# Performance work log

Hardware: AMD Instinct MI355X
Metric: run time of the kernel (lower is better)

The kernel has to match this reference:

```python
import jax, jax.numpy as jnp
import numpy as np

BN_EPS = 1e-5
TN_EPS = 1e-4


def binarize(x):
    # Clipped straight-through binarization (Courbariaux BNN / Brevitas 1-bit):
    # forward = sign(x) in {-1,+1}, backward = hardtanh STE.
    xc = jnp.clip(x, -1.0, 1.0)
    return xc + jax.lax.stop_gradient(jnp.where(x >= 0, 1.0, -1.0).astype(x.dtype) - xc)


def setup_inputs() -> dict:
    key = jax.random.key(0)
    ks = jax.random.split(key, 20)
    B, D, H, C = 16384, 1024, 1024, 10
    inp = {"x": jax.random.uniform(ks[0], (B, D), dtype=jnp.float32)}
    dims = [(H, D), (H, H), (H, H), (C, H)]
    for i, (o, n) in enumerate(dims):
        inp[f"W{i+1}"] = jax.random.uniform(ks[1 + i], (o, n), minval=-1.0, maxval=1.0, dtype=jnp.float32)
    # BatchNorm1d params (eval mode, running stats) for the 3 hidden layers
    for i in range(3):
        k0, k1, k2, k3 = jax.random.split(ks[5 + i], 4)
        inp[f"g{i+1}"] = 1.0 + 0.1 * jax.random.normal(k0, (H,), dtype=jnp.float32)
        inp[f"b{i+1}"] = 0.1 * jax.random.normal(k1, (H,), dtype=jnp.float32)
        inp[f"m{i+1}"] = 0.1 * jax.random.normal(k2, (H,), dtype=jnp.float32)
        inp[f"v{i+1}"] = 0.5 + jax.random.uniform(k3, (H,), dtype=jnp.float32)
    # TensorNorm (scalar norm on the logits)
    inp["tn_w"] = jnp.ones((), dtype=jnp.float32)
    inp["tn_b"] = jnp.zeros((), dtype=jnp.float32)
    inp["tn_m"] = jnp.zeros((), dtype=jnp.float32)
    inp["tn_v"] = jnp.ones((), dtype=jnp.float32)
    return inp


def reference(x, W1, W2, W3, W4,
              g1, b1, m1, v1,
              g2, b2, m2, v2,
              g3, b3, m3, v3,
              tn_w, tn_b, tn_m, tn_v):
    h = binarize(2.0 * x.reshape(x.shape[0], -1) - 1.0)
    # Dropout is identity in eval mode.
    bn = [(g1, b1, m1, v1), (g2, b2, m2, v2), (g3, b3, m3, v3)]
    for W, (g, b, m, v) in zip((W1, W2, W3), bn):
        h = h @ binarize(W).T                      # [B,H] fake-quant linear, no bias
        h = (h - m) * (g * jax.lax.rsqrt(v + BN_EPS)) + b  # BatchNorm1d eval
        h = binarize(h)                            # 1-bit activation quant
    h = h @ binarize(W4).T                         # [B,10]
    # TensorNorm: scalar affine normalization over the whole tensor
    return (h - tn_m) * jax.lax.rsqrt(tn_v + TN_EPS) * tn_w + tn_b
```

## Files before the change

### kernel.cpp

```cpp
#include <hip/hip_runtime.h>
#include <stdint.h>

typedef int  v4i  __attribute__((ext_vector_type(4)));
typedef int  v16i __attribute__((ext_vector_type(16)));
typedef unsigned int uint32;

#define BATCH 16384
#define FEAT  1024

#define OFF_ACTA 0u
#define OFF_ACTB 16777216u
#define OFF_WA1  33554432u
#define OFF_WA2  34603008u
#define OFF_WA3  35651584u
#define OFF_WA4  36700160u
#define OFF_TH   36732928u

__global__ void __launch_bounds__(256) prep_kernel(
    const float* __restrict__ x,
    const float* __restrict__ W1, const float* __restrict__ W2,
    const float* __restrict__ W3, const float* __restrict__ W4,
    const float* __restrict__ g1, const float* __restrict__ b1,
    const float* __restrict__ m1, const float* __restrict__ v1,
    const float* __restrict__ g2, const float* __restrict__ b2,
    const float* __restrict__ m2, const float* __restrict__ v2,
    const float* __restrict__ g3, const float* __restrict__ b3,
    const float* __restrict__ m3, const float* __restrict__ v3,
    char* __restrict__ actA, char* __restrict__ wa1, char* __restrict__ wa2,
    char* __restrict__ wa3, char* __restrict__ wa4, int* __restrict__ TH)
{
    int b = blockIdx.x;
    if (b == 609) {
        for (int gid = threadIdx.x; gid < 3072; gid += 256) {
            int l = gid >> 10, j = gid & 1023;
            const float *g, *bb, *m, *v;
            if (l == 0)      { g = g1; bb = b1; m = m1; v = v1; }
            else if (l == 1) { g = g2; bb = b2; m = m2; v = v2; }
            else             { g = g3; bb = b3; m = m3; v = v3; }
            double gd = (double)g[j], bd = (double)bb[j], md = (double)m[j], vd = (double)v[j];
            double s = gd / sqrt(vd + 1e-5);
            int t2;
            if (s > 0.0)      t2 = (int)ceil(md - bd / s);
            else if (s < 0.0) t2 = -(int)floor(md - bd / s);
            else              t2 = (bd >= 0.0) ? -2000000 : 2000000;
            TH[gid] = t2;
        }
        return;
    }

    const float* src; char* dst; float thr; int nrows; int dblk;
    const float* gp = nullptr;
    if (b < 512)      { src = x  + (size_t)b * 32768;            dst = actA; dblk = b;      thr = 0.5f; nrows = 32; }
    else if (b < 544) { int mb = b - 512; src = W1 + (size_t)mb * 32768; dst = wa1; dblk = mb; thr = 0.0f; nrows = 32; gp = g1; }
    else if (b < 576) { int mb = b - 544; src = W2 + (size_t)mb * 32768; dst = wa2; dblk = mb; thr = 0.0f; nrows = 32; gp = g2; }
    else if (b < 608) { int mb = b - 576; src = W3 + (size_t)mb * 32768; dst = wa3; dblk = mb; thr = 0.0f; nrows = 32; gp = g3; }
    else              { src = W4; dst = wa4; dblk = 0; thr = 0.0f; nrows = 10; }

    __shared__ unsigned char T[32][1040];
#pragma unroll
    for (int u = 0; u < 8; ++u) {
        int unit = threadIdx.x + u * 256;
        int row  = unit >> 6;
        int c16  = (unit & 63) << 4;
        uint32 wb0 = 0, wb1 = 0, wb2 = 0, wb3 = 0;
        if (row < nrows) {
            bool flipb = gp && (gp[dblk * 32 + row] < 0.0f);
            const float* p = src + (size_t)row * 1024 + c16;
            float4 f0 = *(const float4*)(p + 0);
            float4 f1 = *(const float4*)(p + 4);
            float4 f2 = *(const float4*)(p + 8);
            float4 f3 = *(const float4*)(p + 12);
#define BY(f) ((((f) >= thr) != flipb) ? 0x01u : 0xFFu)
            wb0 = BY(f0.x) | (BY(f0.y)<<8) | (BY(f0.z)<<16) | (BY(f0.w)<<24);
            wb1 = BY(f1.x) | (BY(f1.y)<<8) | (BY(f1.z)<<16) | (BY(f1.w)<<24);
            wb2 = BY(f2.x) | (BY(f2.y)<<8) | (BY(f2.z)<<16) | (BY(f2.w)<<24);
            wb3 = BY(f3.x) | (BY(f3.y)<<8) | (BY(f3.z)<<16) | (BY(f3.w)<<24);
#undef BY
        }
        *(uint4*)&T[row][c16] = make_uint4(wb0, wb1, wb2, wb3);
    }
    __syncthreads();

    int lane = threadIdx.x & 63;
    int wv   = threadIdx.x >> 6;
    int row  = lane & 31;
    int hb   = (lane >> 5) * 4;
#pragma unroll
    for (int u = 0; u < 8; ++u) {
        int kk = wv * 8 + u;
        const unsigned char* tr = &T[row][kk * 32 + hb];
        uint32 w0 = *(const uint32*)(tr + 0);
        uint32 w1 = *(const uint32*)(tr + 8);
        uint32 w2 = *(const uint32*)(tr + 16);
        uint32 w3 = *(const uint32*)(tr + 24);
        *(uint4*)(dst + (((size_t)dblk * 32 + kk) * 64 + lane) * 16) = make_uint4(w0, w1, w2, w3);
    }
}

__device__ __forceinline__ void stage_tile(v4i (*Bs)[2048], int bufi,
                                           const v4i* __restrict__ Bin,
                                           int tile, int wv, int lane) {
#pragma unroll
    for (int j = 0; j < 8; ++j) {
        __builtin_amdgcn_global_load_lds(
            (const __attribute__((address_space(1))) void*)
                (Bin + (size_t)tile * 2048 + j * 256 + wv * 64 + lane),
            (__attribute__((address_space(3))) void*)
                (&Bs[bufi][j * 256 + wv * 64]),
            16, 0, 0);
    }
}

__global__ void __launch_bounds__(256, 2) gemm_i8_kernel(
    const v4i* __restrict__ Af, const v4i* __restrict__ Bin,
    const int* __restrict__ th, v4i* __restrict__ Bout)
{
    __shared__ v4i Bs[2][2048];
    __shared__ int Tsh[128];
    const int tid  = threadIdx.x;
    const int lane = tid & 63;
    const int wv   = tid >> 6;
    int bid = blockIdx.x;
    int xcd = bid & 7;
    int i   = bid >> 3;
    int s   = xcd + ((i >> 3) << 3);
    int m   = i & 7;
    int mt  = m * 4 + wv;
    int nb0 = s * 8;

    stage_tile(Bs, 0, Bin, nb0, wv, lane);
    if (tid < 128) Tsh[tid] = th[m * 128 + tid];

    v4i a[32];
    {
        const v4i* Ap = Af + (size_t)mt * 2048;
#pragma unroll
        for (int kk = 0; kk < 32; ++kk) a[kk] = Ap[kk * 64 + lane];
    }
    asm volatile("s_waitcnt vmcnt(0) lgkmcnt(0)" ::: "memory");
    __builtin_amdgcn_s_barrier();

    const int hi4 = (lane >> 5) * 4;
    int buf = 0;
#pragma unroll 1
    for (int it = 0; it < 8; ++it) {
        if (it < 7) stage_tile(Bs, buf ^ 1, Bin, nb0 + it + 1, wv, lane);

        v16i acc0, acc1;
#pragma unroll
        for (int q = 0; q < 16; ++q) {
            acc0[q] = -Tsh[wv * 32 + (q & 3) + 8 * (q >> 2) + hi4];
            acc1[q] = 0;
        }

        v4i b0 = Bs[buf][lane];
        v4i b1 = Bs[buf][16 * 64 + lane];
#pragma unroll
        for (int kk = 0; kk < 16; ++kk) {
            v4i nb0f, nb1f;
            if (kk < 15) {
                nb0f = Bs[buf][(kk + 1) * 64 + lane];
                nb1f = Bs[buf][(kk + 17) * 64 + lane];
            }
            acc0 = __builtin_amdgcn_mfma_i32_32x32x32_i8(a[kk],      b0, acc0, 0, 0, 0);
            acc1 = __builtin_amdgcn_mfma_i32_32x32x32_i8(a[kk + 16], b1, acc1, 0, 0, 0);
            b0 = nb0f; b1 = nb1f;
        }

        uint32 wds0 = 0, wds1 = 0, wds2 = 0, wds3 = 0;
#pragma unroll
        for (int bq = 0; bq < 4; ++bq) {
            { int h = acc0[bq]      + acc1[bq];      wds0 |= (((uint32)((h >> 31) | 1)) & 0xFFu) << (8 * bq); }
            { int h = acc0[4 + bq]  + acc1[4 + bq];  wds1 |= (((uint32)((h >> 31) | 1)) & 0xFFu) << (8 * bq); }
            { int h = acc0[8 + bq]  + acc1[8 + bq];  wds2 |= (((uint32)((h >> 31) | 1)) & 0xFFu) << (8 * bq); }
            { int h = acc0[12 + bq] + acc1[12 + bq]; wds3 |= (((uint32)((h >> 31) | 1)) & 0xFFu) << (8 * bq); }
        }
        v4i ov; ov[0] = (int)wds0; ov[1] = (int)wds1; ov[2] = (int)wds2; ov[3] = (int)wds3;
        Bout[((size_t)(nb0 + it) * 32 + mt) * 64 + lane] = ov;

        if (it < 7) {
            asm volatile("s_waitcnt vmcnt(1)" ::: "memory");
            __builtin_amdgcn_s_barrier();
            buf ^= 1;
        }
    }
}

__global__ void __launch_bounds__(128) final_kernel(
    const v4i* __restrict__ Af4, const v4i* __restrict__ B3,
    const float* __restrict__ tw, const float* __restrict__ tb,
    const float* __restrict__ tm, const float* __restrict__ tv,
    float* __restrict__ out)
{
    int lane = threadIdx.x & 63;
    int nb   = blockIdx.x * 2 + (threadIdx.x >> 6);
    const v4i* Bf = B3 + (size_t)nb * 2048;
    v16i acc;
#pragma unroll
    for (int z = 0; z < 16; ++z) acc[z] = 0;
#pragma unroll
    for (int kk = 0; kk < 32; ++kk) {
        v4i av = Af4[kk * 64 + lane];
        v4i bv = Bf[kk * 64 + lane];
        acc = __builtin_amdgcn_mfma_i32_32x32x32_i8(av, bv, acc, 0, 0, 0);
    }
    double sc  = (double)tw[0] / sqrt((double)tv[0] + 1e-4);
    double off = (double)tb[0] - (double)tm[0] * sc;
    int colg = nb * 32 + (lane & 31);
    int hi   = lane >> 5;
#pragma unroll
    for (int q = 0; q < 8; ++q) {
        int rr = (q & 3) + 8 * (q >> 2) + 4 * hi;
        if (rr < 10)
            out[(size_t)colg * 10 + rr] = (float)((double)acc[q] * sc + off);
    }
}

extern "C" void kernel_launch(void* const* d_in, const int* in_sizes, int n_in,
                              void* d_out, int out_size, void* d_ws, size_t ws_size,
                              hipStream_t stream) {
    const float* x  = (const float*)d_in[0];
    const float* W1 = (const float*)d_in[1];
    const float* W2 = (const float*)d_in[2];
    const float* W3 = (const float*)d_in[3];
    const float* W4 = (const float*)d_in[4];
    const float* g1 = (const float*)d_in[5];
    const float* b1 = (const float*)d_in[6];
    const float* m1 = (const float*)d_in[7];
    const float* v1 = (const float*)d_in[8];
    const float* g2 = (const float*)d_in[9];
    const float* b2 = (const float*)d_in[10];
    const float* m2 = (const float*)d_in[11];
    const float* v2 = (const float*)d_in[12];
    const float* g3 = (const float*)d_in[13];
    const float* b3 = (const float*)d_in[14];
    const float* m3 = (const float*)d_in[15];
    const float* v3 = (const float*)d_in[16];
    const float* tw = (const float*)d_in[17];
    const float* tb = (const float*)d_in[18];
    const float* tm = (const float*)d_in[19];
    const float* tv = (const float*)d_in[20];

    char* ws = (char*)d_ws;
    char* actA = ws + OFF_ACTA;
    char* actB = ws + OFF_ACTB;
    char* wa1  = ws + OFF_WA1;
    char* wa2  = ws + OFF_WA2;
    char* wa3  = ws + OFF_WA3;
    char* wa4  = ws + OFF_WA4;
    int*  TH   = (int*)(ws + OFF_TH);

    prep_kernel<<<610, 256, 0, stream>>>(x, W1, W2, W3, W4,
                                         g1, b1, m1, v1, g2, b2, m2, v2,
                                         g3, b3, m3, v3,
                                         actA, wa1, wa2, wa3, wa4, TH);

    gemm_i8_kernel<<<512, 256, 0, stream>>>((const v4i*)wa1, (const v4i*)actA, TH,        (v4i*)actB);
    gemm_i8_kernel<<<512, 256, 0, stream>>>((const v4i*)wa2, (const v4i*)actB, TH + 1024, (v4i*)actA);
    gemm_i8_kernel<<<512, 256, 0, stream>>>((const v4i*)wa3, (const v4i*)actA, TH + 2048, (v4i*)actB);

    final_kernel<<<256, 128, 0, stream>>>((const v4i*)wa4, (const v4i*)actB,
                                          tw, tb, tm, tv, (float*)d_out);
}
```

Measured before the change: 202.9 us.

## Fuse all binary MLP layers into one persistent kernel keeping activations in LDS

Replaces the three per-layer int8 GEMM launches and the final logits kernel with a single kernel. Each 1024-thread block owns 64 batch rows and keeps their binarized activations in LDS across all layers, streaming the weights from global/L2. Thresholds are pre-permuted so each lane reads them as contiguous int4. This removes the activation round-trips through global memory and three launches. In exchange each block re-reads the full weight matrices for every layer, uses only 256 blocks, and has no prefetch overlap of the weight loads with the MFMAs.

New measurement: 197.9 us. 1.03x faster.

```diff
diff --git a/kernel.cpp b/kernel.cpp
--- a/kernel.cpp
+++ b/kernel.cpp
@@ -43,7 +43,8 @@
             if (s > 0.0)      t2 = (int)ceil(md - bd / s);
             else if (s < 0.0) t2 = -(int)floor(md - bd / s);
             else              t2 = (bd >= 0.0) ? -2000000 : 2000000;
-            TH[gid] = t2;
+            int sidx = (j >> 5) * 32 + ((j >> 2) & 1) * 16 + (j & 3) + 4 * ((j & 31) >> 3);
+            TH[l * 1024 + sidx] = t2;
         }
         return;
     }
@@ -97,122 +98,126 @@
     }
 }
 
-__device__ __forceinline__ void stage_tile(v4i (*Bs)[2048], int bufi,
-                                           const v4i* __restrict__ Bin,
-                                           int tile, int wv, int lane) {
-#pragma unroll
-    for (int j = 0; j < 8; ++j) {
-        __builtin_amdgcn_global_load_lds(
-            (const __attribute__((address_space(1))) void*)
-                (Bin + (size_t)tile * 2048 + j * 256 + wv * 64 + lane),
-            (__attribute__((address_space(3))) void*)
-                (&Bs[bufi][j * 256 + wv * 64]),
-            16, 0, 0);
-    }
-}
-
-__global__ void __launch_bounds__(256, 2) gemm_i8_kernel(
-    const v4i* __restrict__ Af, const v4i* __restrict__ Bin,
-    const int* __restrict__ th, v4i* __restrict__ Bout)
-{
-    __shared__ v4i Bs[2][2048];
-    __shared__ int Tsh[128];
-    const int tid  = threadIdx.x;
-    const int lane = tid & 63;
-    const int wv   = tid >> 6;
-    int bid = blockIdx.x;
-    int xcd = bid & 7;
-    int i   = bid >> 3;
-    int s   = xcd + ((i >> 3) << 3);
-    int m   = i & 7;
-    int mt  = m * 4 + wv;
-    int nb0 = s * 8;
-
-    stage_tile(Bs, 0, Bin, nb0, wv, lane);
-    if (tid < 128) Tsh[tid] = th[m * 128 + tid];
-
-    v4i a[32];
-    {
-        const v4i* Ap = Af + (size_t)mt * 2048;
-#pragma unroll
-        for (int kk = 0; kk < 32; ++kk) a[kk] = Ap[kk * 64 + lane];
-    }
-    asm volatile("s_waitcnt vmcnt(0) lgkmcnt(0)" ::: "memory");
-    __builtin_amdgcn_s_barrier();
-
-    const int hi4 = (lane >> 5) * 4;
-    int buf = 0;
-#pragma unroll 1
-    for (int it = 0; it < 8; ++it) {
-        if (it < 7) stage_tile(Bs, buf ^ 1, Bin, nb0 + it + 1, wv, lane);
-
-        v16i acc0, acc1;
-#pragma unroll
-        for (int q = 0; q < 16; ++q) {
-            acc0[q] = -Tsh[wv * 32 + (q & 3) + 8 * (q >> 2) + hi4];
-            acc1[q] = 0;
-        }
-
-        v4i b0 = Bs[buf][lane];
-        v4i b1 = Bs[buf][16 * 64 + lane];
-#pragma unroll
-        for (int kk = 0; kk < 16; ++kk) {
-            v4i nb0f, nb1f;
-            if (kk < 15) {
-                nb0f = Bs[buf][(kk + 1) * 64 + lane];
-                nb1f = Bs[buf][(kk + 17) * 64 + lane];
-            }
-            acc0 = __builtin_amdgcn_mfma_i32_32x32x32_i8(a[kk],      b0, acc0, 0, 0, 0);
-            acc1 = __builtin_amdgcn_mfma_i32_32x32x32_i8(a[kk + 16], b1, acc1, 0, 0, 0);
-            b0 = nb0f; b1 = nb1f;
-        }
-
-        uint32 wds0 = 0, wds1 = 0, wds2 = 0, wds3 = 0;
-#pragma unroll
-        for (int bq = 0; bq < 4; ++bq) {
-            { int h = acc0[bq]      + acc1[bq];      wds0 |= (((uint32)((h >> 31) | 1)) & 0xFFu) << (8 * bq); }
-            { int h = acc0[4 + bq]  + acc1[4 + bq];  wds1 |= (((uint32)((h >> 31) | 1)) & 0xFFu) << (8 * bq); }
-            { int h = acc0[8 + bq]  + acc1[8 + bq];  wds2 |= (((uint32)((h >> 31) | 1)) & 0xFFu) << (8 * bq); }
-            { int h = acc0[12 + bq] + acc1[12 + bq]; wds3 |= (((uint32)((h >> 31) | 1)) & 0xFFu) << (8 * bq); }
-        }
-        v4i ov; ov[0] = (int)wds0; ov[1] = (int)wds1; ov[2] = (int)wds2; ov[3] = (int)wds3;
-        Bout[((size_t)(nb0 + it) * 32 + mt) * 64 + lane] = ov;
-
-        if (it < 7) {
-            asm volatile("s_waitcnt vmcnt(1)" ::: "memory");
-            __builtin_amdgcn_s_barrier();
-            buf ^= 1;
-        }
-    }
-}
-
-__global__ void __launch_bounds__(128) final_kernel(
-    const v4i* __restrict__ Af4, const v4i* __restrict__ B3,
+__device__ __forceinline__ void gload16(const v4i* gsrc, v4i* ldst) {
+    __builtin_amdgcn_global_load_lds(
+        (const __attribute__((address_space(1))) void*)gsrc,
+        (__attribute__((address_space(3))) void*)ldst, 16, 0, 0);
+}
+
+#define MFMA(a, b, c) __builtin_amdgcn_mfma_i32_32x32x32_i8((a), (b), (c), 0, 0, 0)
+
+__global__ void __launch_bounds__(1024, 4) net_kernel(
+    const v4i* __restrict__ Xp,  const v4i* __restrict__ Wp1,
+    const v4i* __restrict__ Wp2, const v4i* __restrict__ Wp3,
+    const v4i* __restrict__ Wp4, const int* __restrict__ TH,
     const float* __restrict__ tw, const float* __restrict__ tb,
     const float* __restrict__ tm, const float* __restrict__ tv,
     float* __restrict__ out)
 {
-    int lane = threadIdx.x & 63;
-    int nb   = blockIdx.x * 2 + (threadIdx.x >> 6);
-    const v4i* Bf = B3 + (size_t)nb * 2048;
-    v16i acc;
-#pragma unroll
-    for (int z = 0; z < 16; ++z) acc[z] = 0;
-#pragma unroll
-    for (int kk = 0; kk < 32; ++kk) {
-        v4i av = Af4[kk * 64 + lane];
-        v4i bv = Bf[kk * 64 + lane];
-        acc = __builtin_amdgcn_mfma_i32_32x32x32_i8(av, bv, acc, 0, 0, 0);
-    }
-    double sc  = (double)tw[0] / sqrt((double)tv[0] + 1e-4);
-    double off = (double)tb[0] - (double)tm[0] * sc;
-    int colg = nb * 32 + (lane & 31);
-    int hi   = lane >> 5;
-#pragma unroll
-    for (int q = 0; q < 8; ++q) {
-        int rr = (q & 3) + 8 * (q >> 2) + 4 * hi;
-        if (rr < 10)
-            out[(size_t)colg * 10 + rr] = (float)((double)acc[q] * sc + off);
+    __shared__ v4i Hs[4096];
+    const int tid  = threadIdx.x;
+    const int lane = tid & 63;
+    const int wv   = tid >> 6;
+    const int hi   = lane >> 5;
+    const int blk  = blockIdx.x;
+
+    {
+        const v4i* src = Xp + (size_t)blk * 4096;
+#pragma unroll
+        for (int j = 0; j < 4; ++j)
+            gload16(src + j * 1024 + wv * 64 + lane, &Hs[j * 1024 + wv * 64]);
+    }
+    asm volatile("s_waitcnt vmcnt(0)" ::: "memory");
+    __syncthreads();
+
+    const int mt0 = wv * 2, mt1 = wv * 2 + 1;
+    const v4i* Ws[3] = { Wp1, Wp2, Wp3 };
+
+#pragma unroll 1
+    for (int l = 0; l < 3; ++l) {
+        const v4i* W = Ws[l];
+        const int* thl = TH + l * 1024;
+
+        v16i acc00, acc01, acc10, acc11;
+        {
+            const int4* t0 = (const int4*)(thl + mt0 * 32 + hi * 16);
+            const int4* t1 = (const int4*)(thl + mt1 * 32 + hi * 16);
+#pragma unroll
+            for (int g = 0; g < 4; ++g) {
+                int4 ta = t0[g], tc = t1[g];
+                acc00[4*g+0] = -ta.x; acc00[4*g+1] = -ta.y;
+                acc00[4*g+2] = -ta.z; acc00[4*g+3] = -ta.w;
+                acc10[4*g+0] = -tc.x; acc10[4*g+1] = -tc.y;
+                acc10[4*g+2] = -tc.z; acc10[4*g+3] = -tc.w;
+            }
+#pragma unroll
+            for (int q = 0; q < 16; ++q) { acc01[q] = acc00[q]; acc11[q] = acc10[q]; }
+        }
+
+        const v4i* A0 = W + (size_t)mt0 * 2048 + lane;
+        const v4i* A1 = W + (size_t)mt1 * 2048 + lane;
+#pragma unroll 2
+        for (int kk = 0; kk < 32; ++kk) {
+            v4i b0 = Hs[kk * 64 + lane];
+            v4i b1 = Hs[(32 + kk) * 64 + lane];
+            v4i a0 = A0[kk * 64];
+            v4i a1 = A1[kk * 64];
+            acc00 = MFMA(a0, b0, acc00);
+            acc01 = MFMA(a0, b1, acc01);
+            acc10 = MFMA(a1, b0, acc10);
+            acc11 = MFMA(a1, b1, acc11);
+        }
+
+        uint32 w00[4], w01[4], w10[4], w11[4];
+#pragma unroll
+        for (int g = 0; g < 4; ++g) {
+            uint32 d00 = 0, d01 = 0, d10 = 0, d11 = 0;
+#pragma unroll
+            for (int bq = 0; bq < 4; ++bq) {
+                int q = 4 * g + bq;
+                d00 |= (((uint32)((acc00[q] >> 31) | 1)) & 0xFFu) << (8 * bq);
+                d01 |= (((uint32)((acc01[q] >> 31) | 1)) & 0xFFu) << (8 * bq);
+                d10 |= (((uint32)((acc10[q] >> 31) | 1)) & 0xFFu) << (8 * bq);
+                d11 |= (((uint32)((acc11[q] >> 31) | 1)) & 0xFFu) << (8 * bq);
+            }
+            w00[g] = d00; w01[g] = d01; w10[g] = d10; w11[g] = d11;
+        }
+
+        __syncthreads();
+        {
+            v4i o;
+            o[0] = (int)w00[0]; o[1] = (int)w00[1]; o[2] = (int)w00[2]; o[3] = (int)w00[3];
+            Hs[(0 * 32 + mt0) * 64 + lane] = o;
+            o[0] = (int)w01[0]; o[1] = (int)w01[1]; o[2] = (int)w01[2]; o[3] = (int)w01[3];
+            Hs[(32 + mt0) * 64 + lane] = o;
+            o[0] = (int)w10[0]; o[1] = (int)w10[1]; o[2] = (int)w10[2]; o[3] = (int)w10[3];
+            Hs[(0 * 32 + mt1) * 64 + lane] = o;
+            o[0] = (int)w11[0]; o[1] = (int)w11[1]; o[2] = (int)w11[2]; o[3] = (int)w11[3];
+            Hs[(32 + mt1) * 64 + lane] = o;
+        }
+        __syncthreads();
+    }
+
+    if (wv < 2) {
+        const int nb = wv;
+        v16i acc;
+#pragma unroll
+        for (int z = 0; z < 16; ++z) acc[z] = 0;
+#pragma unroll
+        for (int kk = 0; kk < 32; ++kk) {
+            v4i av = Wp4[kk * 64 + lane];
+            v4i bv = Hs[(nb * 32 + kk) * 64 + lane];
+            acc = MFMA(av, bv, acc);
+        }
+        double sc  = (double)tw[0] / sqrt((double)tv[0] + 1e-4);
+        double off = (double)tb[0] - (double)tm[0] * sc;
+        int colg = blk * 64 + nb * 32 + (lane & 31);
+#pragma unroll
+        for (int q = 0; q < 8; ++q) {
+            int rr = (q & 3) + 8 * (q >> 2) + 4 * hi;
+            if (rr < 10)
+                out[(size_t)colg * 10 + rr] = (float)((double)acc[q] * sc + off);
+        }
     }
 }
 
@@ -243,7 +248,6 @@
 
     char* ws = (char*)d_ws;
     char* actA = ws + OFF_ACTA;
-    char* actB = ws + OFF_ACTB;
     char* wa1  = ws + OFF_WA1;
     char* wa2  = ws + OFF_WA2;
     char* wa3  = ws + OFF_WA3;
@@ -255,10 +259,8 @@
                                          g3, b3, m3, v3,
                                          actA, wa1, wa2, wa3, wa4, TH);
 
-    gemm_i8_kernel<<<512, 256, 0, stream>>>((const v4i*)wa1, (const v4i*)actA, TH,        (v4i*)actB);
-    gemm_i8_kernel<<<512, 256, 0, stream>>>((const v4i*)wa2, (const v4i*)actB, TH + 1024, (v4i*)actA);
-    gemm_i8_kernel<<<512, 256, 0, stream>>>((const v4i*)wa3, (const v4i*)actA, TH + 2048, (v4i*)actB);
-
-    final_kernel<<<256, 128, 0, stream>>>((const v4i*)wa4, (const v4i*)actB,
-                                          tw, tb, tm, tv, (float*)d_out);
-}
+    net_kernel<<<256, 1024, 0, stream>>>((const v4i*)actA,
+                                         (const v4i*)wa1, (const v4i*)wa2,
+                                         (const v4i*)wa3, (const v4i*)wa4,
+                                         TH, tw, tb, tm, tv, (float*)d_out);
+}
```
